# Kernel tuning notes

Hardware: AMD Instinct MI355X
Metric: run time of the kernel (lower is better)

Reference implementation:

```python
import jax, jax.numpy as jnp
import numpy as np

EPS = 1e-5

def _conv(x, w, b, dil, pad, groups):
    y = jax.lax.conv_general_dilated(
        x, w, window_strides=(1, 1), padding=[(pad, pad), (pad, pad)],
        rhs_dilation=(dil, dil), dimension_numbers=('NCHW', 'OIHW', 'NCHW'),
        feature_group_count=groups)
    return y + b[None, :, None, None]

def setup_inputs() -> dict:
    key = jax.random.key(0)
    ks = jax.random.split(key, 12)
    B, C, H, W = 16, 128, 128, 128
    half = C // 2  # 64
    x = jax.random.normal(ks[0], (B, C, H, W), dtype=jnp.float32)
    # depthwise 3x3 (groups=half) + pointwise 1x1
    dw_w = jax.random.normal(ks[1], (half, 1, 3, 3), dtype=jnp.float32) * 0.1
    dw_b = jax.random.normal(ks[2], (half,), dtype=jnp.float32) * 0.1
    pw_w = jax.random.normal(ks[3], (half, half, 1, 1), dtype=jnp.float32) * (1.0 / np.sqrt(half))
    pw_b = jax.random.normal(ks[4], (half,), dtype=jnp.float32) * 0.1
    # four 1->1 channel 3x3 convs with dilations 1..4 (weights shared across blocks)
    mcc_w = jax.random.normal(ks[5], (4, 1, 1, 3, 3), dtype=jnp.float32) * 0.2
    mcc_b = jax.random.normal(ks[6], (4,), dtype=jnp.float32) * 0.1
    gamma = jnp.ones((C,), dtype=jnp.float32)
    beta = jnp.zeros((C,), dtype=jnp.float32)
    return {"x": x, "dw_w": dw_w, "dw_b": dw_b, "pw_w": pw_w, "pw_b": pw_b,
            "mcc_w": mcc_w, "mcc_b": mcc_b, "gamma": gamma, "beta": beta}

def reference(x, dw_w, dw_b, pw_w, pw_b, mcc_w, mcc_b, gamma, beta):
    B, C, H, W = x.shape
    half = C // 2
    nblk = half // 4
    # split_channel: even channels -> x1, odd channels -> x2
    x1 = x[:, 0::2]
    x2 = x[:, 1::2]
    # branch 1: depthwise 3x3 then pointwise 1x1
    x1 = _conv(x1, dw_w, dw_b, dil=1, pad=1, groups=half)
    x1 = _conv(x1, pw_w, pw_b, dil=1, pad=0, groups=1)
    # branch 2: channel i of x2 goes through dilated conv (i mod 4); vectorize by
    # gathering channels j::4 and running one depthwise conv per dilation.
    ys = []
    for j in range(4):
        d = j + 1
        xj = x2[:, j::4]                       # [B, nblk, H, W]
        wj = jnp.tile(mcc_w[j], (nblk, 1, 1, 1))  # [nblk,1,3,3] shared kernel
        bj = jnp.tile(mcc_b[j], (nblk,))
        ys.append(_conv(xj, wj, bj, dil=d, pad=d, groups=nblk))
    # interleave back: channel 4*b+j <- ys[j][:, b]
    mcc = jnp.stack(ys, axis=2).reshape(B, half, H, W)
    fusion = jnp.concatenate([x1, mcc], axis=1)  # [B, C, H, W]
    # BatchNorm2d (training mode: batch statistics, biased variance) + ReLU
    mean = jnp.mean(fusion, axis=(0, 2, 3), keepdims=True)
    var = jnp.var(fusion, axis=(0, 2, 3), keepdims=True)
    norm = (fusion - mean) * jax.lax.rsqrt(var + EPS)
    out = norm * gamma[None, :, None, None] + beta[None, :, None, None]
    return jax.nn.relu(out)
```

## Files before the change

### kernel.cpp

```cpp
#include <hip/hip_runtime.h>
#include <hip/hip_bf16.h>

#define Bn 16
#define Cn 128
#define Hn 128
#define Wn 128
#define HWn (Hn*Wn)
#define CHWn (Cn*HWn)
#define HALF 64
#define NTOT (Bn*HWn)

__device__ __forceinline__ float4 fma4(float s, float4 v, float4 a) {
  a.x = fmaf(s, v.x, a.x); a.y = fmaf(s, v.y, a.y);
  a.z = fmaf(s, v.z, a.z); a.w = fmaf(s, v.w, a.w);
  return a;
}
__device__ __forceinline__ unsigned pk2(float a, float b) {
  union { __hip_bfloat162 h; unsigned u; } cv;
  cv.h.x = __float2bfloat16(a); cv.h.y = __float2bfloat16(b);
  return cv.u;
}
__device__ __forceinline__ float2 upk2(unsigned u) {
  union { unsigned u; __hip_bfloat162 h; } cv; cv.u = u;
  return make_float2(__bfloat162float(cv.h.x), __bfloat162float(cv.h.y));
}

__global__ void transpose_pw(const float* __restrict__ pw_w, float* __restrict__ wsT) {
  int i = blockIdx.x*256 + threadIdx.x;
  int co = i >> 6, ki = i & 63;
  wsT[ki*64 + co] = pw_w[i];
}

__device__ __forceinline__ float4 row3(float4 acc, float4 B, float wa, float wb,
                                       float wc, int lane31) {
  float xl = __shfl_up(B.w, 1);
  float xr = __shfl_down(B.x, 1);
  if (lane31 == 0)  xl = 0.f;
  if (lane31 == 31) xr = 0.f;
  float4 L = make_float4(xl, B.x, B.y, B.z);
  float4 R = make_float4(B.y, B.z, B.w, xr);
  acc = fma4(wa, L, acc);
  acc = fma4(wb, B, acc);
  acc = fma4(wc, R, acc);
  return acc;
}

template<bool BF16>
__global__ __launch_bounds__(256, 3) void dwpw_kernel(
    const float* __restrict__ x, const float* __restrict__ wsT,
    const float* __restrict__ dw_w, const float* __restrict__ dw_b,
    const float* __restrict__ pw_b, float* __restrict__ outf,
    __hip_bfloat16* __restrict__ outh, float* __restrict__ stats)
{
  __shared__ float dw_lds[HALF*128];
  __shared__ float wt[HALF*64];
  __shared__ float dww[640];
  __shared__ float sred[128];

  const int t = threadIdx.x;
  const int b = blockIdx.x >> 7;
  const int h = blockIdx.x & 127;

  #pragma unroll
  for (int i = 0; i < 4; ++i)
    ((float4*)wt)[t + 256*i] = ((const float4*)wsT)[t + 256*i];
  for (int i = t; i < 576; i += 256) {
    int k = i / 9, j = i - k*9;
    dww[j*64 + k] = dw_w[i];
  }
  if (t < 64)  dww[576 + t] = dw_b[t];
  if (t < 128) sred[t] = 0.f;
  __syncthreads();

  {
    const int lane31 = t & 31;
    const int px4 = lane31 << 2;
    const int k0 = t >> 5;
    const float* xb = x + (size_t)b*CHWn + (size_t)h*Wn + px4;
    const bool hasU = (h > 0), hasD = (h < Hn-1);
    const float4 z4 = make_float4(0.f,0.f,0.f,0.f);
    #pragma unroll
    for (int i = 0; i < 8; ++i) {
      const int k = k0*8 + i;
      const float* xc = xb + (size_t)(2*k)*HWn;
      float4 r0 = hasU ? *(const float4*)(xc - Wn) : z4;
      float4 r1 = *(const float4*)xc;
      float4 r2 = hasD ? *(const float4*)(xc + Wn) : z4;
      float bk = dww[576 + k];
      float4 a = make_float4(bk, bk, bk, bk);
      a = row3(a, r0, dww[0*64+k], dww[1*64+k], dww[2*64+k], lane31);
      a = row3(a, r1, dww[3*64+k], dww[4*64+k], dww[5*64+k], lane31);
      a = row3(a, r2, dww[6*64+k], dww[7*64+k], dww[8*64+k], lane31);
      *(float4*)&dw_lds[k*128 + px4] = a;
    }
  }
  __syncthreads();

  {
    const int lane = t & 63;
    const int wv   = t >> 6;
    const int cg   = lane & 15;
    const int pg   = lane >> 4;
    const int c0   = cg << 2;
    const int px0  = wv*32 + pg*8;

    float4 bias = *(const float4*)&pw_b[c0];
    float4 aA[4], aB[4];
    aA[0] = make_float4(bias.x, bias.x, bias.x, bias.x); aB[0] = aA[0];
    aA[1] = make_float4(bias.y, bias.y, bias.y, bias.y); aB[1] = aA[1];
    aA[2] = make_float4(bias.z, bias.z, bias.z, bias.z); aB[2] = aA[2];
    aA[3] = make_float4(bias.w, bias.w, bias.w, bias.w); aB[3] = aA[3];

    #pragma unroll 8
    for (int k = 0; k < 64; ++k) {
      float4 wf = *(const float4*)&wt[k*64 + c0];
      float4 dA = *(const float4*)&dw_lds[k*128 + px0];
      float4 dB = *(const float4*)&dw_lds[k*128 + px0 + 4];
      aA[0] = fma4(wf.x, dA, aA[0]); aB[0] = fma4(wf.x, dB, aB[0]);
      aA[1] = fma4(wf.y, dA, aA[1]); aB[1] = fma4(wf.y, dB, aB[1]);
      aA[2] = fma4(wf.z, dA, aA[2]); aB[2] = fma4(wf.z, dB, aB[2]);
      aA[3] = fma4(wf.w, dA, aA[3]); aB[3] = fma4(wf.w, dB, aB[3]);
    }

    const size_t ob = (size_t)b*CHWn + (size_t)h*Wn + px0;
    #pragma unroll
    for (int ci = 0; ci < 4; ++ci) {
      if (BF16) {
        uint4 pk;
        pk.x = pk2(aA[ci].x, aA[ci].y);
        pk.y = pk2(aA[ci].z, aA[ci].w);
        pk.z = pk2(aB[ci].x, aB[ci].y);
        pk.w = pk2(aB[ci].z, aB[ci].w);
        *(uint4*)(outh + ob + (size_t)(c0+ci)*HWn) = pk;
      } else {
        *(float4*)(outf + ob + (size_t)(c0+ci)*HWn)     = aA[ci];
        *(float4*)(outf + ob + (size_t)(c0+ci)*HWn + 4) = aB[ci];
      }
    }

    float s[4], q[4];
    #pragma unroll
    for (int ci = 0; ci < 4; ++ci) {
      float4 u = aA[ci], v = aB[ci];
      s[ci] = (u.x+u.y+u.z+u.w) + (v.x+v.y+v.z+v.w);
      q[ci] = u.x*u.x+u.y*u.y+u.z*u.z+u.w*u.w
            + v.x*v.x+v.y*v.y+v.z*v.z+v.w*v.w;
    }
    #pragma unroll
    for (int ci = 0; ci < 4; ++ci) {
      s[ci] += __shfl_xor(s[ci], 16); s[ci] += __shfl_xor(s[ci], 32);
      q[ci] += __shfl_xor(q[ci], 16); q[ci] += __shfl_xor(q[ci], 32);
    }
    if (pg == 0) {
      #pragma unroll
      for (int ci = 0; ci < 4; ++ci) {
        atomicAdd(&sred[c0+ci], s[ci]);
        atomicAdd(&sred[HALF+c0+ci], q[ci]);
      }
    }
  }
  __syncthreads();
  if (t < HALF)        atomicAdd(&stats[t], sred[t]);
  else if (t < 2*HALF) atomicAdd(&stats[64 + t], sred[t]);
}

template<int D> __device__ __forceinline__ float4 shiftL(float4 A, float4 B) {
  if (D == 1) return make_float4(A.w, B.x, B.y, B.z);
  if (D == 2) return make_float4(A.z, A.w, B.x, B.y);
  if (D == 3) return make_float4(A.y, A.z, A.w, B.x);
  return A;
}
template<int D> __device__ __forceinline__ float4 shiftR(float4 B, float4 C) {
  if (D == 1) return make_float4(B.y, B.z, B.w, C.x);
  if (D == 2) return make_float4(B.z, B.w, C.x, C.y);
  if (D == 3) return make_float4(B.w, C.x, C.y, C.z);
  return C;
}

template<bool BF16, int D>
__device__ __forceinline__ void mcc_compute(
    const float* __restrict__ xc, const float* __restrict__ wj, float bj,
    float* __restrict__ outf, __hip_bfloat16* __restrict__ outh,
    float* lds, int t, int h0, float& s, float& q)
{
  const int R = 16 + 2*D;
  for (int idx = t; idx < R*32; idx += 256) {
    int r = idx >> 5, p4 = (idx & 31) << 2;
    int gr = h0 - D + r;
    float4 v = make_float4(0.f,0.f,0.f,0.f);
    if (gr >= 0 && gr < Hn) v = *(const float4*)(xc + gr*Wn + p4);
    *(float4*)&lds[r*128 + p4] = v;
  }
  __syncthreads();
  const int px4 = (t & 31) << 2;
  const int rl  = t >> 5;
  s = 0.f; q = 0.f;
  #pragma unroll
  for (int rr = 0; rr < 2; ++rr) {
    const int row = rl + rr*8;
    float4 acc = make_float4(bj, bj, bj, bj);
    #pragma unroll
    for (int dr = 0; dr < 3; ++dr) {
      const float* lrow = &lds[(row + dr*D)*128];
      float4 B4 = *(const float4*)(lrow + px4);
      float4 A4 = make_float4(0.f,0.f,0.f,0.f);
      float4 C4 = make_float4(0.f,0.f,0.f,0.f);
      if (px4 > 0)   A4 = *(const float4*)(lrow + px4 - 4);
      if (px4 < 124) C4 = *(const float4*)(lrow + px4 + 4);
      acc = fma4(wj[dr*3+0], shiftL<D>(A4, B4), acc);
      acc = fma4(wj[dr*3+1], B4, acc);
      acc = fma4(wj[dr*3+2], shiftR<D>(B4, C4), acc);
    }
    if (BF16) {
      uint2 pk; pk.x = pk2(acc.x, acc.y); pk.y = pk2(acc.z, acc.w);
      *(uint2*)(outh + (size_t)(h0+row)*Wn + px4) = pk;
    } else {
      *(float4*)(outf + (size_t)(h0+row)*Wn + px4) = acc;
    }
    s += acc.x + acc.y + acc.z + acc.w;
    q += acc.x*acc.x + acc.y*acc.y + acc.z*acc.z + acc.w*acc.w;
  }
}

template<bool BF16>
__global__ __launch_bounds__(256) void mcc_kernel(
    const float* __restrict__ x, const float* __restrict__ mcc_w,
    const float* __restrict__ mcc_b, float* __restrict__ outf,
    __hip_bfloat16* __restrict__ outh, float* __restrict__ stats)
{
  __shared__ float lds[24*128];
  __shared__ float red[8];
  const int t  = threadIdx.x;
  const int hb = blockIdx.x & 7;
  const int m  = (blockIdx.x >> 3) & 63;
  const int b  = blockIdx.x >> 9;
  const int j  = m & 3;
  const int h0 = hb << 4;

  const float* xc = x + (size_t)b*CHWn + (size_t)(2*m+1)*HWn;
  const size_t oo = (size_t)b*CHWn + (size_t)(HALF+m)*HWn;
  float* of = BF16 ? nullptr : outf + oo;
  __hip_bfloat16* oh = BF16 ? outh + oo : nullptr;
  const float* wj = mcc_w + j*9;
  const float bj = mcc_b[j];

  float s = 0.f, q = 0.f;
  switch (j) {
    case 0: mcc_compute<BF16,1>(xc, wj, bj, of, oh, lds, t, h0, s, q); break;
    case 1: mcc_compute<BF16,2>(xc, wj, bj, of, oh, lds, t, h0, s, q); break;
    case 2: mcc_compute<BF16,3>(xc, wj, bj, of, oh, lds, t, h0, s, q); break;
    default: mcc_compute<BF16,4>(xc, wj, bj, of, oh, lds, t, h0, s, q); break;
  }

  #pragma unroll
  for (int off = 32; off > 0; off >>= 1) {
    s += __shfl_down(s, off);
    q += __shfl_down(q, off);
  }
  const int wv = t >> 6;
  if ((t & 63) == 0) { red[wv] = s; red[4+wv] = q; }
  __syncthreads();
  if (t == 0) {
    atomicAdd(&stats[HALF + m],       red[0]+red[1]+red[2]+red[3]);
    atomicAdd(&stats[128 + HALF + m], red[4]+red[5]+red[6]+red[7]);
  }
}

__global__ __launch_bounds__(256) void norm_bf_kernel(
    const __hip_bfloat16* __restrict__ inh, float* __restrict__ out,
    const float* __restrict__ stats, const float* __restrict__ gamma,
    const float* __restrict__ beta)
{
  __shared__ float ssc[128], ssh[128];
  const int t = threadIdx.x;
  if (t < 128) {
    const float n = (float)NTOT;
    float mean = stats[t] / n;
    float var  = stats[128 + t] / n - mean*mean;
    float inv  = 1.0f / sqrtf(var + 1e-5f);
    float sc = gamma[t] * inv;
    ssc[t] = sc;
    ssh[t] = beta[t] - mean * sc;
  }
  __syncthreads();
  const int nq = Bn*CHWn/8;
  const uint4* in = (const uint4*)inh;
  for (int qi = blockIdx.x*256 + t; qi < nq; qi += gridDim.x*256) {
    int c = (qi >> 11) & 127;
    float sc = ssc[c], sh = ssh[c];
    uint4 p = in[qi];
    float2 f0 = upk2(p.x), f1 = upk2(p.y), f2 = upk2(p.z), f3 = upk2(p.w);
    float4 a, bq;
    a.x = fmaxf(fmaf(f0.x, sc, sh), 0.f);
    a.y = fmaxf(fmaf(f0.y, sc, sh), 0.f);
    a.z = fmaxf(fmaf(f1.x, sc, sh), 0.f);
    a.w = fmaxf(fmaf(f1.y, sc, sh), 0.f);
    bq.x = fmaxf(fmaf(f2.x, sc, sh), 0.f);
    bq.y = fmaxf(fmaf(f2.y, sc, sh), 0.f);
    bq.z = fmaxf(fmaf(f3.x, sc, sh), 0.f);
    bq.w = fmaxf(fmaf(f3.y, sc, sh), 0.f);
    *(float4*)(out + (size_t)qi*8)     = a;
    *(float4*)(out + (size_t)qi*8 + 4) = bq;
  }
}

__global__ __launch_bounds__(256) void norm_f32_kernel(float* __restrict__ out,
    const float* __restrict__ stats, const float* __restrict__ gamma,
    const float* __restrict__ beta)
{
  __shared__ float ssc[128], ssh[128];
  const int t = threadIdx.x;
  if (t < 128) {
    const float n = (float)NTOT;
    float mean = stats[t] / n;
    float var  = stats[128 + t] / n - mean*mean;
    float inv  = 1.0f / sqrtf(var + 1e-5f);
    float sc = gamma[t] * inv;
    ssc[t] = sc;
    ssh[t] = beta[t] - mean * sc;
  }
  __syncthreads();
  const int nq = Bn*CHWn/4;
  for (int qi = blockIdx.x*256 + t; qi < nq; qi += gridDim.x*256) {
    int c = (qi >> 12) & 127;
    float sc = ssc[c], sh = ssh[c];
    float4 v = ((const float4*)out)[qi];
    v.x = fmaxf(fmaf(v.x, sc, sh), 0.f);
    v.y = fmaxf(fmaf(v.y, sc, sh), 0.f);
    v.z = fmaxf(fmaf(v.z, sc, sh), 0.f);
    v.w = fmaxf(fmaf(v.w, sc, sh), 0.f);
    ((float4*)out)[qi] = v;
  }
}

extern "C" void kernel_launch(void* const* d_in, const int* in_sizes, int n_in,
                              void* d_out, int out_size, void* d_ws, size_t ws_size,
                              hipStream_t stream)
{
  (void)in_sizes; (void)n_in; (void)out_size;
  const float* x     = (const float*)d_in[0];
  const float* dw_w  = (const float*)d_in[1];
  const float* dw_b  = (const float*)d_in[2];
  const float* pw_w  = (const float*)d_in[3];
  const float* pw_b  = (const float*)d_in[4];
  const float* mcc_w = (const float*)d_in[5];
  const float* mcc_b = (const float*)d_in[6];
  const float* gamma = (const float*)d_in[7];
  const float* beta  = (const float*)d_in[8];
  float* out   = (float*)d_out;
  float* stats = (float*)d_ws;
  float* wsT   = (float*)((char*)d_ws + 1024);
  __hip_bfloat16* bf = (__hip_bfloat16*)((char*)d_ws + 17408);
  const size_t need = 17408 + (size_t)Bn*CHWn*2;
  const bool useBF = ws_size >= need;

  hipMemsetAsync(d_ws, 0, 1024, stream);
  transpose_pw<<<16, 256, 0, stream>>>(pw_w, wsT);
  if (useBF) {
    dwpw_kernel<true><<<Bn*Hn, 256, 0, stream>>>(x, wsT, dw_w, dw_b, pw_b, nullptr, bf, stats);
    mcc_kernel<true><<<Bn*HALF*(Hn/16), 256, 0, stream>>>(x, mcc_w, mcc_b, nullptr, bf, stats);
    norm_bf_kernel<<<8192, 256, 0, stream>>>(bf, out, stats, gamma, beta);
  } else {
    dwpw_kernel<false><<<Bn*Hn, 256, 0, stream>>>(x, wsT, dw_w, dw_b, pw_b, out, nullptr, stats);
    mcc_kernel<false><<<Bn*HALF*(Hn/16), 256, 0, stream>>>(x, mcc_w, mcc_b, out, nullptr, stats);
    norm_f32_kernel<<<8192, 256, 0, stream>>>(out, stats, gamma, beta);
  }
}
```

Measured before the change: 369.8 us.

## Use bf16 MFMA for pointwise conv, drop LDS in mcc, per-plane norm

```diff
diff --git a/kernel.cpp b/kernel.cpp
--- a/kernel.cpp
+++ b/kernel.cpp
@@ -10,25 +10,31 @@
 #define HALF 64
 #define NTOT (Bn*HWn)
 
+#define DT_P 76
+#define WL_P 76
+#define CB_P 136
+
+typedef __attribute__((ext_vector_type(8))) short short8;
+typedef __attribute__((ext_vector_type(4))) float floatx4;
+
 __device__ __forceinline__ float4 fma4(float s, float4 v, float4 a) {
   a.x = fmaf(s, v.x, a.x); a.y = fmaf(s, v.y, a.y);
   a.z = fmaf(s, v.z, a.z); a.w = fmaf(s, v.w, a.w);
   return a;
 }
-__device__ __forceinline__ unsigned pk2(float a, float b) {
-  union { __hip_bfloat162 h; unsigned u; } cv;
-  cv.h.x = __float2bfloat16(a); cv.h.y = __float2bfloat16(b);
-  return cv.u;
-}
-__device__ __forceinline__ float2 upk2(unsigned u) {
-  union { unsigned u; __hip_bfloat162 h; } cv; cv.u = u;
-  return make_float2(__bfloat162float(cv.h.x), __bfloat162float(cv.h.y));
-}
-
-__global__ void transpose_pw(const float* __restrict__ pw_w, float* __restrict__ wsT) {
-  int i = blockIdx.x*256 + threadIdx.x;
-  int co = i >> 6, ki = i & 63;
-  wsT[ki*64 + co] = pw_w[i];
+__device__ __forceinline__ unsigned short f2bf(float f) {
+  union { __hip_bfloat16 h; unsigned short u; } cv;
+  cv.h = __float2bfloat16(f); return cv.u;
+}
+__device__ __forceinline__ float bf2f(unsigned short u) {
+  union { unsigned short u; __hip_bfloat16 h; } cv; cv.u = u;
+  return __bfloat162float(cv.h);
+}
+__device__ __forceinline__ short8 ld_frag(const unsigned short* p) {
+  union { uint2 u[2]; short8 s; } cv;
+  cv.u[0] = *(const uint2*)p;
+  cv.u[1] = *(const uint2*)(p + 4);
+  return cv.s;
 }
 
 __device__ __forceinline__ float4 row3(float4 acc, float4 B, float wa, float wb,
@@ -47,13 +53,13 @@
 
 template<bool BF16>
 __global__ __launch_bounds__(256, 3) void dwpw_kernel(
-    const float* __restrict__ x, const float* __restrict__ wsT,
+    const float* __restrict__ x, const float* __restrict__ pw_w,
     const float* __restrict__ dw_w, const float* __restrict__ dw_b,
     const float* __restrict__ pw_b, float* __restrict__ outf,
     __hip_bfloat16* __restrict__ outh, float* __restrict__ stats)
 {
-  __shared__ float dw_lds[HALF*128];
-  __shared__ float wt[HALF*64];
+  __shared__ unsigned short DtCb[128*DT_P];
+  __shared__ unsigned short Wl[64*WL_P];
   __shared__ float dww[640];
   __shared__ float sred[128];
 
@@ -61,9 +67,14 @@
   const int b = blockIdx.x >> 7;
   const int h = blockIdx.x & 127;
 
-  #pragma unroll
-  for (int i = 0; i < 4; ++i)
-    ((float4*)wt)[t + 256*i] = ((const float4*)wsT)[t + 256*i];
+  for (int i = t; i < 1024; i += 256) {
+    int c = i >> 4, k4 = (i & 15) << 2;
+    float4 w = ((const float4*)pw_w)[i];
+    union { unsigned short us[4]; uint2 u; } cv;
+    cv.us[0] = f2bf(w.x); cv.us[1] = f2bf(w.y);
+    cv.us[2] = f2bf(w.z); cv.us[3] = f2bf(w.w);
+    *(uint2*)&Wl[c*WL_P + k4] = cv.u;
+  }
   for (int i = t; i < 576; i += 256) {
     int k = i / 9, j = i - k*9;
     dww[j*64 + k] = dw_w[i];
@@ -79,6 +90,8 @@
     const float* xb = x + (size_t)b*CHWn + (size_t)h*Wn + px4;
     const bool hasU = (h > 0), hasD = (h < Hn-1);
     const float4 z4 = make_float4(0.f,0.f,0.f,0.f);
+    unsigned pkq[4][4];
+    unsigned lo[4];
     #pragma unroll
     for (int i = 0; i < 8; ++i) {
       const int k = k0*8 + i;
@@ -91,77 +104,128 @@
       a = row3(a, r0, dww[0*64+k], dww[1*64+k], dww[2*64+k], lane31);
       a = row3(a, r1, dww[3*64+k], dww[4*64+k], dww[5*64+k], lane31);
       a = row3(a, r2, dww[6*64+k], dww[7*64+k], dww[8*64+k], lane31);
-      *(float4*)&dw_lds[k*128 + px4] = a;
-    }
-  }
-  __syncthreads();
-
-  {
-    const int lane = t & 63;
-    const int wv   = t >> 6;
-    const int cg   = lane & 15;
-    const int pg   = lane >> 4;
-    const int c0   = cg << 2;
-    const int px0  = wv*32 + pg*8;
-
-    float4 bias = *(const float4*)&pw_b[c0];
-    float4 aA[4], aB[4];
-    aA[0] = make_float4(bias.x, bias.x, bias.x, bias.x); aB[0] = aA[0];
-    aA[1] = make_float4(bias.y, bias.y, bias.y, bias.y); aB[1] = aA[1];
-    aA[2] = make_float4(bias.z, bias.z, bias.z, bias.z); aB[2] = aA[2];
-    aA[3] = make_float4(bias.w, bias.w, bias.w, bias.w); aB[3] = aA[3];
-
-    #pragma unroll 8
-    for (int k = 0; k < 64; ++k) {
-      float4 wf = *(const float4*)&wt[k*64 + c0];
-      float4 dA = *(const float4*)&dw_lds[k*128 + px0];
-      float4 dB = *(const float4*)&dw_lds[k*128 + px0 + 4];
-      aA[0] = fma4(wf.x, dA, aA[0]); aB[0] = fma4(wf.x, dB, aB[0]);
-      aA[1] = fma4(wf.y, dA, aA[1]); aB[1] = fma4(wf.y, dB, aB[1]);
-      aA[2] = fma4(wf.z, dA, aA[2]); aB[2] = fma4(wf.z, dB, aB[2]);
-      aA[3] = fma4(wf.w, dA, aA[3]); aB[3] = fma4(wf.w, dB, aB[3]);
-    }
-
-    const size_t ob = (size_t)b*CHWn + (size_t)h*Wn + px0;
-    #pragma unroll
-    for (int ci = 0; ci < 4; ++ci) {
-      if (BF16) {
-        uint4 pk;
-        pk.x = pk2(aA[ci].x, aA[ci].y);
-        pk.y = pk2(aA[ci].z, aA[ci].w);
-        pk.z = pk2(aB[ci].x, aB[ci].y);
-        pk.w = pk2(aB[ci].z, aB[ci].w);
-        *(uint4*)(outh + ob + (size_t)(c0+ci)*HWn) = pk;
+      float av[4] = {a.x, a.y, a.z, a.w};
+      if ((i & 1) == 0) {
+        #pragma unroll
+        for (int j = 0; j < 4; ++j) lo[j] = f2bf(av[j]);
       } else {
-        *(float4*)(outf + ob + (size_t)(c0+ci)*HWn)     = aA[ci];
-        *(float4*)(outf + ob + (size_t)(c0+ci)*HWn + 4) = aB[ci];
+        #pragma unroll
+        for (int j = 0; j < 4; ++j)
+          pkq[j][i>>1] = lo[j] | ((unsigned)f2bf(av[j]) << 16);
       }
     }
-
-    float s[4], q[4];
-    #pragma unroll
-    for (int ci = 0; ci < 4; ++ci) {
-      float4 u = aA[ci], v = aB[ci];
-      s[ci] = (u.x+u.y+u.z+u.w) + (v.x+v.y+v.z+v.w);
-      q[ci] = u.x*u.x+u.y*u.y+u.z*u.z+u.w*u.w
-            + v.x*v.x+v.y*v.y+v.z*v.z+v.w*v.w;
+    #pragma unroll
+    for (int j = 0; j < 4; ++j) {
+      unsigned short* p = &DtCb[(px4+j)*DT_P + k0*8];
+      uint2 w0; w0.x = pkq[j][0]; w0.y = pkq[j][1];
+      uint2 w1; w1.x = pkq[j][2]; w1.y = pkq[j][3];
+      *(uint2*)p       = w0;
+      *(uint2*)(p + 4) = w1;
     }
-    #pragma unroll
-    for (int ci = 0; ci < 4; ++ci) {
-      s[ci] += __shfl_xor(s[ci], 16); s[ci] += __shfl_xor(s[ci], 32);
-      q[ci] += __shfl_xor(q[ci], 16); q[ci] += __shfl_xor(q[ci], 32);
+  }
+  __syncthreads();
+
+  const int lane = t & 63;
+  const int wv   = t >> 6;
+  const int q4   = lane >> 4;
+  const int n16  = lane & 15;
+
+  short8 Af[4][2], Bf[2][2];
+  #pragma unroll
+  for (int ct = 0; ct < 4; ++ct)
+    #pragma unroll
+    for (int kc = 0; kc < 2; ++kc)
+      Af[ct][kc] = ld_frag(&Wl[(ct*16 + n16)*WL_P + kc*32 + q4*8]);
+  #pragma unroll
+  for (int nt = 0; nt < 2; ++nt)
+    #pragma unroll
+    for (int kc = 0; kc < 2; ++kc)
+      Bf[nt][kc] = ld_frag(&DtCb[(wv*32 + nt*16 + n16)*DT_P + kc*32 + q4*8]);
+
+  floatx4 C[4][2];
+  #pragma unroll
+  for (int ct = 0; ct < 4; ++ct) {
+    float4 bs = *(const float4*)&pw_b[ct*16 + q4*4];
+    floatx4 ini = {bs.x, bs.y, bs.z, bs.w};
+    C[ct][0] = ini; C[ct][1] = ini;
+  }
+  #pragma unroll
+  for (int kc = 0; kc < 2; ++kc)
+    #pragma unroll
+    for (int ct = 0; ct < 4; ++ct)
+      #pragma unroll
+      for (int nt = 0; nt < 2; ++nt)
+        C[ct][nt] = __builtin_amdgcn_mfma_f32_16x16x32_bf16(
+            Af[ct][kc], Bf[nt][kc], C[ct][nt], 0, 0, 0);
+
+  __syncthreads();
+
+  {
+    float S[4][4], Q[4][4];
+    #pragma unroll
+    for (int ct = 0; ct < 4; ++ct)
+      #pragma unroll
+      for (int r = 0; r < 4; ++r) {
+        float a = C[ct][0][r], c2 = C[ct][1][r];
+        S[ct][r] = a + c2;
+        Q[ct][r] = a*a + c2*c2;
+      }
+    #pragma unroll
+    for (int off = 1; off < 16; off <<= 1)
+      #pragma unroll
+      for (int ct = 0; ct < 4; ++ct)
+        #pragma unroll
+        for (int r = 0; r < 4; ++r) {
+          S[ct][r] += __shfl_xor(S[ct][r], off);
+          Q[ct][r] += __shfl_xor(Q[ct][r], off);
+        }
+    if (n16 == 0) {
+      #pragma unroll
+      for (int ct = 0; ct < 4; ++ct)
+        #pragma unroll
+        for (int r = 0; r < 4; ++r) {
+          int c = ct*16 + q4*4 + r;
+          atomicAdd(&sred[c], S[ct][r]);
+          atomicAdd(&sred[64 + c], Q[ct][r]);
+        }
     }
-    if (pg == 0) {
-      #pragma unroll
-      for (int ci = 0; ci < 4; ++ci) {
-        atomicAdd(&sred[c0+ci], s[ci]);
-        atomicAdd(&sred[HALF+c0+ci], q[ci]);
-      }
+  }
+
+  const size_t ob = (size_t)b*CHWn + (size_t)h*Wn;
+  if (BF16) {
+    #pragma unroll
+    for (int ct = 0; ct < 4; ++ct)
+      #pragma unroll
+      for (int nt = 0; nt < 2; ++nt)
+        #pragma unroll
+        for (int r = 0; r < 4; ++r) {
+          int c  = ct*16 + q4*4 + r;
+          int px = wv*32 + nt*16 + n16;
+          DtCb[c*CB_P + px] = f2bf(C[ct][nt][r]);
+        }
+  } else {
+    #pragma unroll
+    for (int ct = 0; ct < 4; ++ct)
+      #pragma unroll
+      for (int nt = 0; nt < 2; ++nt)
+        #pragma unroll
+        for (int r = 0; r < 4; ++r) {
+          int c  = ct*16 + q4*4 + r;
+          int px = wv*32 + nt*16 + n16;
+          outf[ob + (size_t)c*HWn + px] = C[ct][nt][r];
+        }
+  }
+  __syncthreads();
+
+  if (BF16) {
+    for (int i = t; i < 1024; i += 256) {
+      int c = i >> 4, p8 = (i & 15) << 3;
+      uint4 v = *(const uint4*)&DtCb[c*CB_P + p8];
+      *(uint4*)(outh + ob + (size_t)c*HWn + p8) = v;
     }
   }
-  __syncthreads();
-  if (t < HALF)        atomicAdd(&stats[t], sred[t]);
-  else if (t < 2*HALF) atomicAdd(&stats[64 + t], sred[t]);
+  if (t < 64)       atomicAdd(&stats[t], sred[t]);
+  else if (t < 128) atomicAdd(&stats[64 + t], sred[t]);
 }
 
 template<int D> __device__ __forceinline__ float4 shiftL(float4 A, float4 B) {
@@ -178,48 +242,36 @@
 }
 
 template<bool BF16, int D>
-__device__ __forceinline__ void mcc_compute(
+__device__ __forceinline__ void mcc_row(
     const float* __restrict__ xc, const float* __restrict__ wj, float bj,
     float* __restrict__ outf, __hip_bfloat16* __restrict__ outh,
-    float* lds, int t, int h0, float& s, float& q)
-{
-  const int R = 16 + 2*D;
-  for (int idx = t; idx < R*32; idx += 256) {
-    int r = idx >> 5, p4 = (idx & 31) << 2;
-    int gr = h0 - D + r;
-    float4 v = make_float4(0.f,0.f,0.f,0.f);
-    if (gr >= 0 && gr < Hn) v = *(const float4*)(xc + gr*Wn + p4);
-    *(float4*)&lds[r*128 + p4] = v;
-  }
-  __syncthreads();
-  const int px4 = (t & 31) << 2;
-  const int rl  = t >> 5;
-  s = 0.f; q = 0.f;
-  #pragma unroll
-  for (int rr = 0; rr < 2; ++rr) {
-    const int row = rl + rr*8;
-    float4 acc = make_float4(bj, bj, bj, bj);
-    #pragma unroll
-    for (int dr = 0; dr < 3; ++dr) {
-      const float* lrow = &lds[(row + dr*D)*128];
-      float4 B4 = *(const float4*)(lrow + px4);
-      float4 A4 = make_float4(0.f,0.f,0.f,0.f);
-      float4 C4 = make_float4(0.f,0.f,0.f,0.f);
-      if (px4 > 0)   A4 = *(const float4*)(lrow + px4 - 4);
-      if (px4 < 124) C4 = *(const float4*)(lrow + px4 + 4);
-      acc = fma4(wj[dr*3+0], shiftL<D>(A4, B4), acc);
-      acc = fma4(wj[dr*3+1], B4, acc);
-      acc = fma4(wj[dr*3+2], shiftR<D>(B4, C4), acc);
+    int h, int px4, float& s, float& q)
+{
+  const float4 z4 = make_float4(0.f,0.f,0.f,0.f);
+  float4 acc = make_float4(bj, bj, bj, bj);
+  #pragma unroll
+  for (int dr = 0; dr < 3; ++dr) {
+    int rr = h + (dr-1)*D;
+    if (rr >= 0 && rr < Hn) {
+      const float* rp = xc + rr*Wn;
+      float4 Bc = *(const float4*)(rp + px4);
+      float4 Ac = (px4 > 0)   ? *(const float4*)(rp + px4 - 4) : z4;
+      float4 Cc = (px4 < 124) ? *(const float4*)(rp + px4 + 4) : z4;
+      acc = fma4(wj[dr*3+0], shiftL<D>(Ac, Bc), acc);
+      acc = fma4(wj[dr*3+1], Bc, acc);
+      acc = fma4(wj[dr*3+2], shiftR<D>(Bc, Cc), acc);
     }
-    if (BF16) {
-      uint2 pk; pk.x = pk2(acc.x, acc.y); pk.y = pk2(acc.z, acc.w);
-      *(uint2*)(outh + (size_t)(h0+row)*Wn + px4) = pk;
-    } else {
-      *(float4*)(outf + (size_t)(h0+row)*Wn + px4) = acc;
-    }
-    s += acc.x + acc.y + acc.z + acc.w;
-    q += acc.x*acc.x + acc.y*acc.y + acc.z*acc.z + acc.w*acc.w;
-  }
+  }
+  if (BF16) {
+    uint2 pk;
+    pk.x = (unsigned)f2bf(acc.x) | ((unsigned)f2bf(acc.y) << 16);
+    pk.y = (unsigned)f2bf(acc.z) | ((unsigned)f2bf(acc.w) << 16);
+    *(uint2*)(outh + (size_t)h*Wn + px4) = pk;
+  } else {
+    *(float4*)(outf + (size_t)h*Wn + px4) = acc;
+  }
+  s = acc.x + acc.y + acc.z + acc.w;
+  q = acc.x*acc.x + acc.y*acc.y + acc.z*acc.z + acc.w*acc.w;
 }
 
 template<bool BF16>
@@ -228,14 +280,14 @@
     const float* __restrict__ mcc_b, float* __restrict__ outf,
     __hip_bfloat16* __restrict__ outh, float* __restrict__ stats)
 {
-  __shared__ float lds[24*128];
   __shared__ float red[8];
   const int t  = threadIdx.x;
-  const int hb = blockIdx.x & 7;
-  const int m  = (blockIdx.x >> 3) & 63;
-  const int b  = blockIdx.x >> 9;
+  const int hb = blockIdx.x & 15;
+  const int m  = (blockIdx.x >> 4) & 63;
+  const int b  = blockIdx.x >> 10;
   const int j  = m & 3;
-  const int h0 = hb << 4;
+  const int h  = (hb << 3) + (t >> 5);
+  const int px4 = (t & 31) << 2;
 
   const float* xc = x + (size_t)b*CHWn + (size_t)(2*m+1)*HWn;
   const size_t oo = (size_t)b*CHWn + (size_t)(HALF+m)*HWn;
@@ -246,10 +298,10 @@
 
   float s = 0.f, q = 0.f;
   switch (j) {
-    case 0: mcc_compute<BF16,1>(xc, wj, bj, of, oh, lds, t, h0, s, q); break;
-    case 1: mcc_compute<BF16,2>(xc, wj, bj, of, oh, lds, t, h0, s, q); break;
-    case 2: mcc_compute<BF16,3>(xc, wj, bj, of, oh, lds, t, h0, s, q); break;
-    default: mcc_compute<BF16,4>(xc, wj, bj, of, oh, lds, t, h0, s, q); break;
+    case 0:  mcc_row<BF16,1>(xc, wj, bj, of, oh, h, px4, s, q); break;
+    case 1:  mcc_row<BF16,2>(xc, wj, bj, of, oh, h, px4, s, q); break;
+    case 2:  mcc_row<BF16,3>(xc, wj, bj, of, oh, h, px4, s, q); break;
+    default: mcc_row<BF16,4>(xc, wj, bj, of, oh, h, px4, s, q); break;
   }
 
   #pragma unroll
@@ -257,8 +309,8 @@
     s += __shfl_down(s, off);
     q += __shfl_down(q, off);
   }
-  const int wv = t >> 6;
-  if ((t & 63) == 0) { red[wv] = s; red[4+wv] = q; }
+  const int wvi = t >> 6;
+  if ((t & 63) == 0) { red[wvi] = s; red[4+wvi] = q; }
   __syncthreads();
   if (t == 0) {
     atomicAdd(&stats[HALF + m],       red[0]+red[1]+red[2]+red[3]);
@@ -267,40 +319,35 @@
 }
 
 __global__ __launch_bounds__(256) void norm_bf_kernel(
-    const __hip_bfloat16* __restrict__ inh, float* __restrict__ out,
+    const unsigned short* __restrict__ inh, float* __restrict__ out,
     const float* __restrict__ stats, const float* __restrict__ gamma,
     const float* __restrict__ beta)
 {
-  __shared__ float ssc[128], ssh[128];
-  const int t = threadIdx.x;
-  if (t < 128) {
-    const float n = (float)NTOT;
-    float mean = stats[t] / n;
-    float var  = stats[128 + t] / n - mean*mean;
-    float inv  = 1.0f / sqrtf(var + 1e-5f);
-    float sc = gamma[t] * inv;
-    ssc[t] = sc;
-    ssh[t] = beta[t] - mean * sc;
-  }
-  __syncthreads();
-  const int nq = Bn*CHWn/8;
-  const uint4* in = (const uint4*)inh;
-  for (int qi = blockIdx.x*256 + t; qi < nq; qi += gridDim.x*256) {
-    int c = (qi >> 11) & 127;
-    float sc = ssc[c], sh = ssh[c];
-    uint4 p = in[qi];
-    float2 f0 = upk2(p.x), f1 = upk2(p.y), f2 = upk2(p.z), f3 = upk2(p.w);
+  const int plane = blockIdx.x;
+  const int c = plane & 127;
+  const float n = (float)NTOT;
+  float mean = stats[c] / n;
+  float var  = stats[128 + c] / n - mean*mean;
+  float sc = gamma[c] / sqrtf(var + 1e-5f);
+  float sh = beta[c] - mean * sc;
+
+  const uint4* in = (const uint4*)(inh + (size_t)plane*HWn);
+  float* op = out + (size_t)plane*HWn;
+  #pragma unroll
+  for (int i = 0; i < 8; ++i) {
+    int idx = threadIdx.x + i*256;
+    uint4 p = in[idx];
     float4 a, bq;
-    a.x = fmaxf(fmaf(f0.x, sc, sh), 0.f);
-    a.y = fmaxf(fmaf(f0.y, sc, sh), 0.f);
-    a.z = fmaxf(fmaf(f1.x, sc, sh), 0.f);
-    a.w = fmaxf(fmaf(f1.y, sc, sh), 0.f);
-    bq.x = fmaxf(fmaf(f2.x, sc, sh), 0.f);
-    bq.y = fmaxf(fmaf(f2.y, sc, sh), 0.f);
-    bq.z = fmaxf(fmaf(f3.x, sc, sh), 0.f);
-    bq.w = fmaxf(fmaf(f3.y, sc, sh), 0.f);
-    *(float4*)(out + (size_t)qi*8)     = a;
-    *(float4*)(out + (size_t)qi*8 + 4) = bq;
+    a.x = fmaxf(fmaf(bf2f(p.x & 0xffff), sc, sh), 0.f);
+    a.y = fmaxf(fmaf(bf2f(p.x >> 16),    sc, sh), 0.f);
+    a.z = fmaxf(fmaf(bf2f(p.y & 0xffff), sc, sh), 0.f);
+    a.w = fmaxf(fmaf(bf2f(p.y >> 16),    sc, sh), 0.f);
+    bq.x = fmaxf(fmaf(bf2f(p.z & 0xffff), sc, sh), 0.f);
+    bq.y = fmaxf(fmaf(bf2f(p.z >> 16),    sc, sh), 0.f);
+    bq.z = fmaxf(fmaf(bf2f(p.w & 0xffff), sc, sh), 0.f);
+    bq.w = fmaxf(fmaf(bf2f(p.w >> 16),    sc, sh), 0.f);
+    *(float4*)(op + idx*8)     = a;
+    *(float4*)(op + idx*8 + 4) = bq;
   }
 }
 
@@ -308,28 +355,23 @@
     const float* __restrict__ stats, const float* __restrict__ gamma,
     const float* __restrict__ beta)
 {
-  __shared__ float ssc[128], ssh[128];
-  const int t = threadIdx.x;
-  if (t < 128) {
-    const float n = (float)NTOT;
-    float mean = stats[t] / n;
-    float var  = stats[128 + t] / n - mean*mean;
-    float inv  = 1.0f / sqrtf(var + 1e-5f);
-    float sc = gamma[t] * inv;
-    ssc[t] = sc;
-    ssh[t] = beta[t] - mean * sc;
-  }
-  __syncthreads();
-  const int nq = Bn*CHWn/4;
-  for (int qi = blockIdx.x*256 + t; qi < nq; qi += gridDim.x*256) {
-    int c = (qi >> 12) & 127;
-    float sc = ssc[c], sh = ssh[c];
-    float4 v = ((const float4*)out)[qi];
+  const int plane = blockIdx.x;
+  const int c = plane & 127;
+  const float n = (float)NTOT;
+  float mean = stats[c] / n;
+  float var  = stats[128 + c] / n - mean*mean;
+  float sc = gamma[c] / sqrtf(var + 1e-5f);
+  float sh = beta[c] - mean * sc;
+  float* op = out + (size_t)plane*HWn;
+  #pragma unroll
+  for (int i = 0; i < 16; ++i) {
+    int idx = threadIdx.x + i*256;
+    float4 v = ((const float4*)op)[idx];
     v.x = fmaxf(fmaf(v.x, sc, sh), 0.f);
     v.y = fmaxf(fmaf(v.y, sc, sh), 0.f);
     v.z = fmaxf(fmaf(v.z, sc, sh), 0.f);
     v.w = fmaxf(fmaf(v.w, sc, sh), 0.f);
-    ((float4*)out)[qi] = v;
+    ((float4*)op)[idx] = v;
   }
 }
 
@@ -349,20 +391,18 @@
   const float* beta  = (const float*)d_in[8];
   float* out   = (float*)d_out;
   float* stats = (float*)d_ws;
-  float* wsT   = (float*)((char*)d_ws + 1024);
-  __hip_bfloat16* bf = (__hip_bfloat16*)((char*)d_ws + 17408);
-  const size_t need = 17408 + (size_t)Bn*CHWn*2;
+  __hip_bfloat16* bf = (__hip_bfloat16*)((char*)d_ws + 1024);
+  const size_t need = 1024 + (size_t)Bn*CHWn*2;
   const bool useBF = ws_size >= need;
 
   hipMemsetAsync(d_ws, 0, 1024, stream);
-  transpose_pw<<<16, 256, 0, stream>>>(pw_w, wsT);
   if (useBF) {
-    dwpw_kernel<true><<<Bn*Hn, 256, 0, stream>>>(x, wsT, dw_w, dw_b, pw_b, nullptr, bf, stats);
-    mcc_kernel<true><<<Bn*HALF*(Hn/16), 256, 0, stream>>>(x, mcc_w, mcc_b, nullptr, bf, stats);
-    norm_bf_kernel<<<8192, 256, 0, stream>>>(bf, out, stats, gamma, beta);
+    dwpw_kernel<true><<<Bn*Hn, 256, 0, stream>>>(x, pw_w, dw_w, dw_b, pw_b, nullptr, bf, stats);
+    mcc_kernel<true><<<Bn*HALF*(Hn/8), 256, 0, stream>>>(x, mcc_w, mcc_b, nullptr, bf, stats);
+    norm_bf_kernel<<<Bn*Cn, 256, 0, stream>>>((const unsigned short*)bf, out, stats, gamma, beta);
   } else {
-    dwpw_kernel<false><<<Bn*Hn, 256, 0, stream>>>(x, wsT, dw_w, dw_b, pw_b, out, nullptr, stats);
-    mcc_kernel<false><<<Bn*HALF*(Hn/16), 256, 0, stream>>>(x, mcc_w, mcc_b, out, nullptr, stats);
-    norm_f32_kernel<<<8192, 256, 0, stream>>>(out, stats, gamma, beta);
-  }
-}
+    dwpw_kernel<false><<<Bn*Hn, 256, 0, stream>>>(x, pw_w, dw_w, dw_b, pw_b, out, nullptr, stats);
+    mcc_kernel<false><<<Bn*HALF*(Hn/8), 256, 0, stream>>>(x, mcc_w, mcc_b, out, nullptr, stats);
+    norm_f32_kernel<<<Bn*Cn, 256, 0, stream>>>(out, stats, gamma, beta);
+  }
+}
```

Measured after the change: 462.8 us. 25.2% more time.
